# Optimization experiments

Hardware: AMD Instinct MI355X
Metric: run time of the kernel (lower is better)

Reference implementation:

```python
import jax, jax.numpy as jnp
import numpy as np

DECAY = 0.8
CODEBOOK_SIZE = 8192
DIM = 256
NORM_EPS = 1e-12  # matches F.normalize default eps


def _l2norm(t):
    n = jnp.linalg.norm(t, axis=-1, keepdims=True)
    return t / jnp.clip(n, NORM_EPS)


def setup_inputs() -> dict:
    key = jax.random.key(0)
    k1, k2 = jax.random.split(key)
    x = jax.random.normal(k1, (8, 2048, DIM), dtype=jnp.float32)
    # non-kmeans init: codebook is a row-normalized gaussian
    embed = _l2norm(jax.random.normal(k2, (CODEBOOK_SIZE, DIM), dtype=jnp.float32))
    return {"x": x, "embed": embed}


def reference(x, embed):
    shape = x.shape
    K = embed.shape[0]
    flatten = x.reshape(-1, shape[-1])            # [N, d]
    fn = _l2norm(flatten)                          # normalized inputs
    en = _l2norm(embed)                            # normalized codebook

    dist = fn @ en.T                               # [N, K] cosine sims
    ind = jnp.argmax(dist, axis=-1)                # [N]

    embed_ind = ind.reshape(shape[:-1])            # [...]
    quantize = embed[embed_ind]                    # gather from RAW codebook, [..., d]

    # training EMA update (onehot matmul expressed as scatter-reduce)
    bins = jax.ops.segment_sum(jnp.ones_like(ind, dtype=x.dtype), ind, num_segments=K)  # [K]
    embed_sum = jax.ops.segment_sum(fn, ind, num_segments=K)                            # [K, d]
    zero_mask = bins == 0
    bins_safe = jnp.where(zero_mask, jnp.asarray(1.0, x.dtype), bins)
    embed_normalized = _l2norm(embed_sum / bins_safe[:, None])
    embed_normalized = jnp.where(zero_mask[:, None], en, embed_normalized)
    embed_new = DECAY * embed + (1.0 - DECAY) * embed_normalized

    return quantize, embed_ind, embed_new
```

## Files before the change

### kernel.cpp

```cpp
#include <hip/hip_runtime.h>
#include <math.h>

#define DIM 256
#define NROWS_TILE 128
#define SPLITS 8
#define CODES_PER_SPLIT 1024
#define CCH 32
#define NPH (CODES_PER_SPLIT / CCH)
#define BUF_F16 8192
#define DELTA 2.2e-3f
#define MAXR 32

typedef __attribute__((ext_vector_type(8))) _Float16 f16x8;
typedef __attribute__((ext_vector_type(4))) _Float16 f16x4;
typedef __attribute__((ext_vector_type(4))) float f32x4;

__device__ __forceinline__ void gload16(const void* g, void* l) {
    __builtin_amdgcn_global_load_lds(
        (const __attribute__((address_space(1))) void*)g,
        (__attribute__((address_space(3))) void*)l, 16, 0, 0);
}

__device__ __forceinline__ float waveReduceSum(float v) {
#pragma unroll
    for (int off = 32; off >= 1; off >>= 1) v += __shfl_xor(v, off, 64);
    return v;
}

__global__ __launch_bounds__(256) void k_prep_all(
    const float* __restrict__ x, const float* __restrict__ embed,
    _Float16* __restrict__ fnh, _Float16* __restrict__ enh,
    float* __restrict__ xnorm, float* __restrict__ enorm,
    float* __restrict__ zero_region, int nzero4, int N, int K)
{
    const int w = threadIdx.x >> 6, lane = threadIdx.x & 63;
    const int r = blockIdx.x * 4 + w;

    const int gid = blockIdx.x * 256 + threadIdx.x;
    if (gid < nzero4)
        *(f32x4*)&zero_region[(size_t)gid * 4] = (f32x4){0.f, 0.f, 0.f, 0.f};

    if (r >= N + K) return;
    const bool isX = (r < N);
    const float* src = isX ? &x[(size_t)r * DIM] : &embed[(size_t)(r - N) * DIM];
    f32x4 v = *(const f32x4*)&src[lane * 4];
    float ss = waveReduceSum(v[0]*v[0] + v[1]*v[1] + v[2]*v[2] + v[3]*v[3]);
    const float n = fmaxf(sqrtf(ss), 1e-12f);
    if (lane == 0) { if (isX) xnorm[r] = n; else enorm[r - N] = n; }
    f16x4 h;
#pragma unroll
    for (int c = 0; c < 4; ++c) h[c] = (_Float16)(v[c] / n);
    _Float16* dst = isX ? &fnh[(size_t)r * DIM] : &enh[(size_t)(r - N) * DIM];
    *(f16x4*)&dst[lane * 4] = h;
}

__global__ __launch_bounds__(256, 2) void k_gemm(
    const _Float16* __restrict__ fnh, const _Float16* __restrict__ enh,
    float* __restrict__ cand_val, int* __restrict__ cand_idx)
{
    __shared__ _Float16 smem[2][BUF_F16];

    const int t = threadIdx.x;
    const int w = t >> 6, lane = t & 63;
    const int rbase = blockIdx.x * NROWS_TILE;
    const int cbase = blockIdx.y * CODES_PER_SPLIT;
    const int koff = (lane >> 4) * 8;

    f16x8 Ah[2][8];
    {
        const size_t arow = (size_t)(rbase + w * 32 + (lane & 15)) * DIM;
#pragma unroll
        for (int i = 0; i < 2; ++i)
#pragma unroll
            for (int kc = 0; kc < 8; ++kc)
                Ah[i][kc] = *(const f16x8*)&fnh[arow + (size_t)i * 16 * DIM + kc * 32 + koff];
    }
    asm volatile("s_waitcnt vmcnt(0)" ::: "memory");

    const int chbase = (w >> 1) * 16;
    const int kcb = (w & 1) * 4;
    const int dstoff = w * 2048;
    const _Float16* gptr = enh + (size_t)(cbase + chbase + (lane & 15)) * DIM + kcb * 32 + koff;

    float v1[2][4], v2[2][4];
    int   c1[2][4], c2[2][4];
#pragma unroll
    for (int i = 0; i < 2; ++i)
#pragma unroll
        for (int rg = 0; rg < 4; ++rg) {
            v1[i][rg] = -2.0f; v2[i][rg] = -2.5f;
            c1[i][rg] = 0;     c2[i][rg] = 0;
        }

    const f32x4 ZERO4 = (f32x4){0.f, 0.f, 0.f, 0.f};

    {
        _Float16* l0 = &smem[0][dstoff];
#pragma unroll
        for (int q = 0; q < 4; ++q)
            gload16(gptr + q * 32, l0 + q * 512);
        gptr += CCH * DIM;
    }

#pragma unroll 1
    for (int c = 0; c < NPH; ++c) {
        const int buf = c & 1;
        asm volatile("s_waitcnt vmcnt(0)" ::: "memory");
        __builtin_amdgcn_s_barrier();
        if (c + 1 < NPH) {
            _Float16* l0 = &smem[buf ^ 1][dstoff];
#pragma unroll
            for (int q = 0; q < 4; ++q)
                gload16(gptr + q * 32, l0 + q * 512);
            gptr += CCH * DIM;
        }

        const _Float16* bufp = &smem[buf][0];
        f32x4 acc[2][2];

#pragma unroll
        for (int s = 0; s < 16; ++s) {
            const int ch = s >> 3;
            const int kc = s & 7;
            const f16x8 Bh = *(const f16x8*)(bufp + s * 512 + lane * 8);
            if (kc == 0) {
#pragma unroll
                for (int i = 0; i < 2; ++i)
                    acc[ch][i] = __builtin_amdgcn_mfma_f32_16x16x32_f16(Ah[i][0], Bh, ZERO4, 0, 0, 0);
            } else {
#pragma unroll
                for (int i = 0; i < 2; ++i)
                    acc[ch][i] = __builtin_amdgcn_mfma_f32_16x16x32_f16(Ah[i][kc], Bh, acc[ch][i], 0, 0, 0);
            }
        }

        const int cb = cbase + c * CCH;
#pragma unroll
        for (int ch = 0; ch < 2; ++ch)
#pragma unroll
            for (int i = 0; i < 2; ++i)
#pragma unroll
                for (int rg = 0; rg < 4; ++rg) {
                    const float vv = acc[ch][i][rg];
                    const int cd = cb + ch * 16;
                    const bool gt1 = vv > v1[i][rg];
                    const bool gt2 = vv > v2[i][rg];
                    const float nv2 = gt1 ? v1[i][rg] : (gt2 ? vv : v2[i][rg]);
                    const int   nc2 = gt1 ? c1[i][rg] : (gt2 ? cd : c2[i][rg]);
                    v2[i][rg] = nv2; c2[i][rg] = nc2;
                    v1[i][rg] = gt1 ? vv : v1[i][rg];
                    c1[i][rg] = gt1 ? cd : c1[i][rg];
                }
    }

#pragma unroll
    for (int i = 0; i < 2; ++i)
#pragma unroll
        for (int rg = 0; rg < 4; ++rg) {
            float lv1 = v1[i][rg], lv2 = v2[i][rg];
            int   li1 = c1[i][rg] + (lane & 15);
            int   li2 = c2[i][rg] + (lane & 15);
            const int r = rbase + w * 32 + i * 16 + (lane >> 4) * 4 + rg;
            const size_t base = ((size_t)r * SPLITS + blockIdx.y) * 4;
#pragma unroll
            for (int p = 0; p < 4; ++p) {
                float mv = lv1; int mi = li1;
#pragma unroll
                for (int off = 1; off < 16; off <<= 1) {
                    const float ov = __shfl_xor(mv, off, 16);
                    const int oi = __shfl_xor(mi, off, 16);
                    if (ov > mv || (ov == mv && oi < mi)) { mv = ov; mi = oi; }
                }
                if ((lane & 15) == 0) {
                    cand_val[base + p] = mv;
                    cand_idx[base + p] = mi;
                }
                if (li1 == mi) {
                    lv1 = lv2; li1 = li2;
                    lv2 = -3e30f; li2 = 0x7fffffff;
                }
            }
        }
}

__global__ __launch_bounds__(256) void k_merge(
    const float* __restrict__ x, const float* __restrict__ embed,
    const float* __restrict__ cand_val, const int* __restrict__ cand_idx,
    const float* __restrict__ xnorm, const float* __restrict__ enorm,
    float* __restrict__ quantize, float* __restrict__ ind_out,
    float* __restrict__ embed_sum, float* __restrict__ bins,
    int* __restrict__ rowlist)
{
    const int w = threadIdx.x >> 6, lane = threadIdx.x & 63;
    const int r = blockIdx.x * 4 + w;
    const int NC = SPLITS * 4;

    float lv = -3e30f; int li = 0x7fffffff;
    if (lane < NC) {
        lv = cand_val[(size_t)r * NC + lane];
        li = cand_idx[(size_t)r * NC + lane];
    }
    float tv[4]; int ti[4];
#pragma unroll
    for (int p = 0; p < 4; ++p) {
        float mv = lv; int mi = li;
#pragma unroll
        for (int off = 1; off < 32; off <<= 1) {
            const float ov = __shfl_xor(mv, off, 32);
            const int oi = __shfl_xor(mi, off, 32);
            if (ov > mv || (ov == mv && oi < mi)) { mv = ov; mi = oi; }
        }
        mv = __shfl(mv, 0, 64);
        mi = __shfl(mi, 0, 64);
        tv[p] = mv; ti[p] = mi;
        if (li == mi) { lv = -3e30f; li = 0x7fffffff; }
    }

    const float xn = xnorm[r];

    int ind;
    if (tv[1] < tv[0] - DELTA) {
        ind = ti[0];
    } else {
        const f32x4 xv4 = *(const f32x4*)&x[(size_t)r * DIM + lane * 4];
        float bv = -3e30f; int bi = 0x7fffffff;
#pragma unroll
        for (int p = 0; p < 4; ++p) {
            if (tv[p] >= tv[0] - DELTA) {
                const int idx = ti[p];
                const f32x4 ev = *(const f32x4*)&embed[(size_t)idx * DIM + lane * 4];
                const float d = xv4[0]*ev[0] + xv4[1]*ev[1] + xv4[2]*ev[2] + xv4[3]*ev[3];
                const float s = waveReduceSum(d);
                const float exact = s / (xn * enorm[idx]);
                if (exact > bv || (exact == bv && idx < bi)) { bv = exact; bi = idx; }
            }
        }
        ind = bi;
    }

    int slot = 0;
    if (lane == 0) {
        ind_out[r] = (float)ind;
        slot = (int)atomicAdd(&bins[ind], 1.0f);
        if (slot < MAXR) rowlist[ind * MAXR + slot] = r;
    }
    slot = __shfl(slot, 0, 64);

    const f32x4 e = *(const f32x4*)&embed[(size_t)ind * DIM + lane * 4];
    *(f32x4*)&quantize[(size_t)r * DIM + lane * 4] = e;

    if (slot >= MAXR) {
        const f32x4 xv4 = *(const f32x4*)&x[(size_t)r * DIM + lane * 4];
        atomicAdd(&embed_sum[(size_t)ind * DIM + lane * 4 + 0], xv4[0] / xn);
        atomicAdd(&embed_sum[(size_t)ind * DIM + lane * 4 + 1], xv4[1] / xn);
        atomicAdd(&embed_sum[(size_t)ind * DIM + lane * 4 + 2], xv4[2] / xn);
        atomicAdd(&embed_sum[(size_t)ind * DIM + lane * 4 + 3], xv4[3] / xn);
    }
}

__global__ __launch_bounds__(256) void k_update(
    const float* __restrict__ x, const float* __restrict__ xnorm,
    const int* __restrict__ rowlist, const float* __restrict__ bins,
    const float* __restrict__ embed, const float* __restrict__ embed_sum,
    float* __restrict__ embed_new, int K)
{
    const int w = threadIdx.x >> 6, lane = threadIdx.x & 63;
    const int k = blockIdx.x * 4 + w;
    if (k >= K) return;

    const float bcnt = bins[k];
    const int cnt = (int)bcnt;

    f32x4 s = (f32x4){0.f, 0.f, 0.f, 0.f};
    if (cnt > MAXR)
        s = *(const f32x4*)&embed_sum[(size_t)k * DIM + lane * 4];

    const int nl = (cnt < MAXR) ? cnt : MAXR;
    for (int j = 0; j < nl; ++j) {
        const int r = rowlist[k * MAXR + j];
        const f32x4 xv = *(const f32x4*)&x[(size_t)r * DIM + lane * 4];
        const float xn = xnorm[r];
#pragma unroll
        for (int c = 0; c < 4; ++c) s[c] += xv[c] / xn;
    }

    f32x4 e = *(const f32x4*)&embed[(size_t)k * DIM + lane * 4];
    float sse = waveReduceSum(e[0]*e[0] + e[1]*e[1] + e[2]*e[2] + e[3]*e[3]);
    const float ne = fmaxf(sqrtf(sse), 1e-12f);

    const float bs = (cnt == 0) ? 1.f : bcnt;
    f32x4 vv;
#pragma unroll
    for (int c = 0; c < 4; ++c) vv[c] = s[c] / bs;
    float ssv = waveReduceSum(vv[0]*vv[0] + vv[1]*vv[1] + vv[2]*vv[2] + vv[3]*vv[3]);
    const float nv = fmaxf(sqrtf(ssv), 1e-12f);

    f32x4 o;
#pragma unroll
    for (int c = 0; c < 4; ++c) {
        const float norm_c = (cnt == 0) ? (e[c] / ne) : (vv[c] / nv);
        o[c] = 0.8f * e[c] + 0.2f * norm_c;
    }
    *(f32x4*)&embed_new[(size_t)k * DIM + lane * 4] = o;
}

extern "C" void kernel_launch(void* const* d_in, const int* in_sizes, int n_in,
                              void* d_out, int out_size, void* d_ws, size_t ws_size,
                              hipStream_t stream) {
    const float* x = (const float*)d_in[0];
    const float* embed = (const float*)d_in[1];
    const int N = in_sizes[0] / DIM;
    const int K = in_sizes[1] / DIM;

    float* quantize  = (float*)d_out;
    float* ind_out   = quantize + (size_t)N * DIM;
    float* embed_new = ind_out + N;

    char* ws = (char*)d_ws;
    _Float16* fnh = (_Float16*)ws;
    _Float16* enh = (_Float16*)(ws + (size_t)N * DIM * 2);
    char* p = ws + (size_t)N * DIM * 2 + (size_t)K * DIM * 2;
    float* xnorm    = (float*)p;                 p += (size_t)N * 4;
    float* enorm    = (float*)p;                 p += (size_t)K * 4;
    float* cand_val = (float*)p;                 p += (size_t)N * SPLITS * 4 * 4;
    int*   cand_idx = (int*)p;                   p += (size_t)N * SPLITS * 4 * 4;
    int*   rowlist  = (int*)p;                   p += (size_t)K * MAXR * 4;
    float* embed_sum = (float*)p;
    float* bins      = embed_sum + (size_t)K * DIM;
    const int nzero4 = (K * DIM + K) / 4;

    k_prep_all<<<(N + K + 3) / 4, 256, 0, stream>>>(x, embed, fnh, enh, xnorm,
                                                    enorm, embed_sum, nzero4, N, K);

    dim3 grid(N / NROWS_TILE, SPLITS);
    k_gemm<<<grid, 256, 0, stream>>>(fnh, enh, cand_val, cand_idx);

    k_merge<<<(N + 3) / 4, 256, 0, stream>>>(x, embed, cand_val, cand_idx, xnorm,
                                             enorm, quantize, ind_out, embed_sum,
                                             bins, rowlist);
    k_update<<<(K + 3) / 4, 256, 0, stream>>>(x, xnorm, rowlist, bins, embed,
                                              embed_sum, embed_new, K);
}
```

Baseline: 134.1 us.

## Replace direct global-to-LDS loads with register-staged two-deep prefetch pipeline

Replaces the global_load_lds copies of codebook tiles with ordinary global loads into registers, issued two phases ahead and written to the double-buffered LDS after the current phase's MFMA and argmax work. The main loop is unrolled by two with alternating register buffers, so each barrier waits only on LDS writes (lgkmcnt) rather than draining all outstanding global loads (vmcnt). This is meant to hide global memory latency behind compute, at the cost of extra VGPRs for the staging registers and an explicit LDS store pass.

```diff
diff --git a/kernel.cpp b/kernel.cpp
--- a/kernel.cpp
+++ b/kernel.cpp
@@ -15,12 +15,6 @@
 typedef __attribute__((ext_vector_type(4))) _Float16 f16x4;
 typedef __attribute__((ext_vector_type(4))) float f32x4;
 
-__device__ __forceinline__ void gload16(const void* g, void* l) {
-    __builtin_amdgcn_global_load_lds(
-        (const __attribute__((address_space(1))) void*)g,
-        (__attribute__((address_space(3))) void*)l, 16, 0, 0);
-}
-
 __device__ __forceinline__ float waveReduceSum(float v) {
 #pragma unroll
     for (int off = 32; off >= 1; off >>= 1) v += __shfl_xor(v, off, 64);
@@ -75,7 +69,6 @@
             for (int kc = 0; kc < 8; ++kc)
                 Ah[i][kc] = *(const f16x8*)&fnh[arow + (size_t)i * 16 * DIM + kc * 32 + koff];
     }
-    asm volatile("s_waitcnt vmcnt(0)" ::: "memory");
 
     const int chbase = (w >> 1) * 16;
     const int kcb = (w & 1) * 4;
@@ -94,64 +87,79 @@
 
     const f32x4 ZERO4 = (f32x4){0.f, 0.f, 0.f, 0.f};
 
+    f16x8 ra[4], rb[4];
+
     {
-        _Float16* l0 = &smem[0][dstoff];
+#pragma unroll
+        for (int q = 0; q < 4; ++q) ra[q] = *(const f16x8*)(gptr + q * 32);
+        gptr += CCH * DIM;
 #pragma unroll
         for (int q = 0; q < 4; ++q)
-            gload16(gptr + q * 32, l0 + q * 512);
+            *(f16x8*)&smem[0][dstoff + q * 512 + lane * 8] = ra[q];
+#pragma unroll
+        for (int q = 0; q < 4; ++q) ra[q] = *(const f16x8*)(gptr + q * 32);
         gptr += CCH * DIM;
-    }
+        asm volatile("s_waitcnt lgkmcnt(0)" ::: "memory");
+        __builtin_amdgcn_s_barrier();
+    }
+
+#define PHASE(C, RW, RI) do {                                                     \
+        if ((C) + 2 < NPH) {                                                      \
+            _Pragma("unroll")                                                     \
+            for (int q = 0; q < 4; ++q) RI[q] = *(const f16x8*)(gptr + q * 32);   \
+            gptr += CCH * DIM;                                                    \
+        }                                                                         \
+        const _Float16* bufp = &smem[(C) & 1][0];                                 \
+        f32x4 acc[2][2];                                                          \
+        _Pragma("unroll")                                                         \
+        for (int s = 0; s < 16; ++s) {                                            \
+            const int ch = s >> 3;                                                \
+            const int kc = s & 7;                                                 \
+            const f16x8 Bh = *(const f16x8*)(bufp + s * 512 + lane * 8);          \
+            if (kc == 0) {                                                        \
+                _Pragma("unroll")                                                 \
+                for (int i = 0; i < 2; ++i)                                       \
+                    acc[ch][i] = __builtin_amdgcn_mfma_f32_16x16x32_f16(          \
+                        Ah[i][0], Bh, ZERO4, 0, 0, 0);                            \
+            } else {                                                              \
+                _Pragma("unroll")                                                 \
+                for (int i = 0; i < 2; ++i)                                       \
+                    acc[ch][i] = __builtin_amdgcn_mfma_f32_16x16x32_f16(          \
+                        Ah[i][kc], Bh, acc[ch][i], 0, 0, 0);                      \
+            }                                                                     \
+        }                                                                         \
+        const int cb = cbase + (C) * CCH;                                         \
+        _Pragma("unroll")                                                         \
+        for (int ch = 0; ch < 2; ++ch)                                            \
+        { _Pragma("unroll")                                                       \
+          for (int i = 0; i < 2; ++i)                                             \
+          { _Pragma("unroll")                                                     \
+            for (int rg = 0; rg < 4; ++rg) {                                      \
+                const float vv = acc[ch][i][rg];                                  \
+                const int cd = cb + ch * 16;                                      \
+                const bool gt1 = vv > v1[i][rg];                                  \
+                const bool gt2 = vv > v2[i][rg];                                  \
+                const float nv2 = gt1 ? v1[i][rg] : (gt2 ? vv : v2[i][rg]);       \
+                const int   nc2 = gt1 ? c1[i][rg] : (gt2 ? cd : c2[i][rg]);       \
+                v2[i][rg] = nv2; c2[i][rg] = nc2;                                 \
+                v1[i][rg] = gt1 ? vv : v1[i][rg];                                 \
+                c1[i][rg] = gt1 ? cd : c1[i][rg];                                 \
+            } } }                                                                 \
+        if ((C) + 1 < NPH) {                                                      \
+            _Pragma("unroll")                                                     \
+            for (int q = 0; q < 4; ++q)                                           \
+                *(f16x8*)&smem[((C) + 1) & 1][dstoff + q * 512 + lane * 8] = RW[q]; \
+            asm volatile("s_waitcnt lgkmcnt(0)" ::: "memory");                    \
+            __builtin_amdgcn_s_barrier();                                         \
+        }                                                                         \
+    } while (0)
 
 #pragma unroll 1
-    for (int c = 0; c < NPH; ++c) {
-        const int buf = c & 1;
-        asm volatile("s_waitcnt vmcnt(0)" ::: "memory");
-        __builtin_amdgcn_s_barrier();
-        if (c + 1 < NPH) {
-            _Float16* l0 = &smem[buf ^ 1][dstoff];
-#pragma unroll
-            for (int q = 0; q < 4; ++q)
-                gload16(gptr + q * 32, l0 + q * 512);
-            gptr += CCH * DIM;
-        }
-
-        const _Float16* bufp = &smem[buf][0];
-        f32x4 acc[2][2];
-
-#pragma unroll
-        for (int s = 0; s < 16; ++s) {
-            const int ch = s >> 3;
-            const int kc = s & 7;
-            const f16x8 Bh = *(const f16x8*)(bufp + s * 512 + lane * 8);
-            if (kc == 0) {
-#pragma unroll
-                for (int i = 0; i < 2; ++i)
-                    acc[ch][i] = __builtin_amdgcn_mfma_f32_16x16x32_f16(Ah[i][0], Bh, ZERO4, 0, 0, 0);
-            } else {
-#pragma unroll
-                for (int i = 0; i < 2; ++i)
-                    acc[ch][i] = __builtin_amdgcn_mfma_f32_16x16x32_f16(Ah[i][kc], Bh, acc[ch][i], 0, 0, 0);
-            }
-        }
-
-        const int cb = cbase + c * CCH;
-#pragma unroll
-        for (int ch = 0; ch < 2; ++ch)
-#pragma unroll
-            for (int i = 0; i < 2; ++i)
-#pragma unroll
-                for (int rg = 0; rg < 4; ++rg) {
-                    const float vv = acc[ch][i][rg];
-                    const int cd = cb + ch * 16;
-                    const bool gt1 = vv > v1[i][rg];
-                    const bool gt2 = vv > v2[i][rg];
-                    const float nv2 = gt1 ? v1[i][rg] : (gt2 ? vv : v2[i][rg]);
-                    const int   nc2 = gt1 ? c1[i][rg] : (gt2 ? cd : c2[i][rg]);
-                    v2[i][rg] = nv2; c2[i][rg] = nc2;
-                    v1[i][rg] = gt1 ? vv : v1[i][rg];
-                    c1[i][rg] = gt1 ? cd : c1[i][rg];
-                }
-    }
+    for (int cc = 0; cc < NPH; cc += 2) {
+        PHASE(cc, ra, rb);
+        PHASE(cc + 1, rb, ra);
+    }
+#undef PHASE
 
 #pragma unroll
     for (int i = 0; i < 2; ++i)
```

New measurement: 150.1 us. 1.12x slower.
